# Optimization experiments

Hardware: AMD Instinct MI355X
Metric: run time of the kernel (lower is better)

## Reference

```python
import jax, jax.numpy as jnp
import numpy as np

N, M, D = 32768, 8192, 64

def setup_inputs() -> dict:
    key = jax.random.key(0)
    k1, k2, k3 = jax.random.split(key, 3)
    inputx = jax.random.normal(k1, (N, D), dtype=jnp.float32)
    y = jax.random.normal(k2, (M, D), dtype=jnp.float32)
    # psi is initialized to zeros in the module, but use random values so the
    # dual-variable subtraction actually affects the argmin/min.
    psi = jax.random.normal(k3, (M,), dtype=jnp.float32)
    return {"inputx": inputx, "y": y, "psi": psi}

def reference(inputx, y, psi):
    # cxy[i,j] = ||x_i||^2 + ||y_j||^2 - 2 <x_i, y_j>   (squared euclidean cost)
    x2 = jnp.sum(inputx * inputx, axis=1, keepdims=True)          # [N,1]
    y2 = jnp.sum(y * y, axis=1)[None, :]                          # [1,M]
    cxy = x2 + y2 - 2.0 * jnp.matmul(inputx, y.T)                 # [N,M]
    # semi-dual: mean_i min_j (c(x_i,y_j) - psi_j) + mean_j psi_j
    loss = jnp.mean(jnp.min(cxy - psi[None, :], axis=1)) + jnp.mean(psi)
    return loss
```

## Files before the change

### kernel.cpp

```cpp
#include <hip/hip_runtime.h>

#define N_ROWS 32768
#define M_COLS 8192
#define D_DIM  64
#define JC     8
#define BLOCK  256
#define ROWS_PER_BLOCK 256
#define CHUNK  (M_COLS / JC)
#define TJ     128
#define NTILE  (CHUNK / TJ)

typedef _Float16 v8h __attribute__((ext_vector_type(8)));
typedef _Float16 v4h __attribute__((ext_vector_type(4)));
typedef float    v4f __attribute__((ext_vector_type(4)));

__global__ __launch_bounds__(BLOCK) void prep_kernel(
    const float* __restrict__ y, const float* __restrict__ psi,
    _Float16* __restrict__ yh, float* __restrict__ th) {
    const int tid = threadIdx.x;
    const int j = blockIdx.x * 16 + (tid >> 4);
    const int n = tid & 15;
    const float4 v = *(const float4*)(y + (size_t)j * D_DIM + n * 4);
    float s = v.x * v.x + v.y * v.y + v.z * v.z + v.w * v.w;
    v4h hv = { (_Float16)v.x, (_Float16)v.y, (_Float16)v.z, (_Float16)v.w };
    *(v4h*)(yh + (size_t)j * D_DIM + n * 4) = hv;
#pragma unroll
    for (int m = 1; m < 16; m <<= 1) s += __shfl_xor(s, m, 64);
    if (n == 0) th[j] = 0.5f * (psi[j] - s);
}

__global__ __launch_bounds__(BLOCK) void partial_min_kernel(
    const float* __restrict__ x, const _Float16* __restrict__ yh,
    const float* __restrict__ th, float* __restrict__ part) {
    __shared__ __align__(16) _Float16 sY[2][TJ * D_DIM];

    const int tid  = threadIdx.x;
    const int lane = tid & 63, wave = tid >> 6;
    const int q = lane >> 4, n = lane & 15;
    const int jc    = blockIdx.y;
    const int jbase = jc * CHUNK;
    const int i_wave = blockIdx.x * ROWS_PER_BLOCK + wave * 64;

    v8h a[4][2];
#pragma unroll
    for (int g = 0; g < 4; ++g) {
        const float* px = x + (size_t)(i_wave + g * 16 + n) * D_DIM + q * 8;
#pragma unroll
        for (int c = 0; c < 2; ++c) {
            float4 f0 = *(const float4*)(px + c * 32);
            float4 f1 = *(const float4*)(px + c * 32 + 4);
            v8h av = { (_Float16)f0.x, (_Float16)f0.y, (_Float16)f0.z, (_Float16)f0.w,
                       (_Float16)f1.x, (_Float16)f1.y, (_Float16)f1.z, (_Float16)f1.w };
            a[g][c] = av;
        }
    }

    float maxs[4][4];
#pragma unroll
    for (int g = 0; g < 4; ++g)
#pragma unroll
        for (int r = 0; r < 4; ++r) maxs[g][r] = -INFINITY;

    auto stage = [&](int t, int b) {
#pragma unroll
        for (int k = 0; k < 4; ++k) {
            const int sIdx = (k * 4 + wave) * 64 + lane;
            const int row  = sIdx >> 3;
            const int c    = (sIdx & 7) ^ (row & 7);
            const _Float16* g = yh + (size_t)(jbase + t * TJ + row) * D_DIM + c * 8;
            __builtin_amdgcn_global_load_lds(
                (const __attribute__((address_space(1))) void*)g,
                (__attribute__((address_space(3))) void*)(&sY[b][(size_t)(k * 4 + wave) * 512]),
                16, 0, 0);
        }
    };

    stage(0, 0);
    __syncthreads();

    const int sl0 = q ^ (n & 7);

    for (int t = 0; t < NTILE; ++t) {
        const int cur = t & 1;
        if (t + 1 < NTILE) stage(t + 1, cur ^ 1);

        const _Float16* buf = &sY[cur][0];
        const float* pt = th + jbase + t * TJ + n;
#pragma unroll 2
        for (int ss = 0; ss < TJ / 16; ++ss) {
            const v8h b0 = *(const v8h*)(buf + (ss * 16 + n) * 64 + sl0 * 8);
            const v8h b1 = *(const v8h*)(buf + (ss * 16 + n) * 64 + (sl0 ^ 4) * 8);
            const float tv = pt[ss * 16];
            const v4f tv4 = { tv, tv, tv, tv };
#pragma unroll
            for (int g = 0; g < 4; ++g) {
                v4f acc = __builtin_amdgcn_mfma_f32_16x16x32_f16(a[g][0], b0, tv4, 0, 0, 0);
                acc     = __builtin_amdgcn_mfma_f32_16x16x32_f16(a[g][1], b1, acc, 0, 0, 0);
#pragma unroll
                for (int r = 0; r < 4; ++r)
                    maxs[g][r] = fmaxf(maxs[g][r], acc[r]);
            }
        }
        __syncthreads();
    }

#pragma unroll
    for (int g = 0; g < 4; ++g) {
#pragma unroll
        for (int r = 0; r < 4; ++r) {
            float v = maxs[g][r];
#pragma unroll
            for (int m = 1; m < 16; m <<= 1)
                v = fmaxf(v, __shfl_xor(v, m, 64));
            if (n == 0)
                part[(size_t)jc * N_ROWS + i_wave + g * 16 + q * 4 + r] = -2.f * v;
        }
    }
}

__global__ __launch_bounds__(BLOCK) void reduce_kernel(
    const float* __restrict__ part, const float* __restrict__ x,
    const float* __restrict__ psi, float* __restrict__ out) {
    const int tid = threadIdx.x;
    const int gt  = blockIdx.x * BLOCK + tid;
    float m = part[gt];
#pragma unroll
    for (int c = 1; c < JC; ++c)
        m = fminf(m, part[(size_t)c * N_ROWS + gt]);
    float s = m;
    const float4* xv = (const float4*)x;
    float x2 = 0.f;
#pragma unroll
    for (int k = 0; k < 16; ++k) {
        float4 v = xv[gt + k * 32768];
        x2 += v.x * v.x + v.y * v.y + v.z * v.z + v.w * v.w;
    }
    s = (s + x2) * (1.f / (float)N_ROWS);
    if (gt < M_COLS) s += psi[gt] * (1.f / (float)M_COLS);
    for (int off = 32; off > 0; off >>= 1) s += __shfl_down(s, off, 64);
    __shared__ float tmp[4];
    if ((tid & 63) == 0) tmp[tid >> 6] = s;
    __syncthreads();
    if (tid == 0) atomicAdd(out, tmp[0] + tmp[1] + tmp[2] + tmp[3]);
}

extern "C" void kernel_launch(void* const* d_in, const int* in_sizes, int n_in,
                              void* d_out, int out_size, void* d_ws, size_t ws_size,
                              hipStream_t stream) {
    const float* x   = (const float*)d_in[0];
    const float* y   = (const float*)d_in[1];
    const float* psi = (const float*)d_in[2];
    float* out = (float*)d_out;

    float* part = (float*)d_ws;
    float* th   = part + (size_t)JC * N_ROWS;
    _Float16* yh = (_Float16*)(th + M_COLS);

    hipMemsetAsync(out, 0, sizeof(float), stream);
    prep_kernel<<<M_COLS / 16, BLOCK, 0, stream>>>(y, psi, yh, th);
    partial_min_kernel<<<dim3(N_ROWS / ROWS_PER_BLOCK, JC), BLOCK, 0, stream>>>(x, yh, th, part);
    reduce_kernel<<<N_ROWS / BLOCK, BLOCK, 0, stream>>>(part, x, psi, out);
}
```

Measured before the change: 121.9 us.

## Double rows per wave, stage theta in LDS, fold output zeroing into prep

Each wave now processes 128 rows (8 MFMA groups) instead of 64, so every Y tile loaded into LDS feeds twice as many MFMAs and the block count halves. The per-column theta values are copied into LDS alongside Y through global_load_lds instead of being read from global memory inside the inner loop, and the inner loop is unrolled further. The hipMemsetAsync on the output is replaced by a store inside prep_kernel, which removes one launch. The cost is higher register pressure from doubled A fragments and accumulators, and only 512 blocks in the grid, which may reduce occupancy and leave some CUs idle.

```diff
diff --git a/kernel.cpp b/kernel.cpp
--- a/kernel.cpp
+++ b/kernel.cpp
@@ -5,7 +5,8 @@
 #define D_DIM  64
 #define JC     8
 #define BLOCK  256
-#define ROWS_PER_BLOCK 256
+#define GROUPS 8
+#define ROWS_PER_BLOCK 512
 #define CHUNK  (M_COLS / JC)
 #define TJ     128
 #define NTILE  (CHUNK / TJ)
@@ -16,8 +17,9 @@
 
 __global__ __launch_bounds__(BLOCK) void prep_kernel(
     const float* __restrict__ y, const float* __restrict__ psi,
-    _Float16* __restrict__ yh, float* __restrict__ th) {
+    _Float16* __restrict__ yh, float* __restrict__ th, float* __restrict__ out) {
     const int tid = threadIdx.x;
+    if (blockIdx.x == 0 && tid == 0) out[0] = 0.f;
     const int j = blockIdx.x * 16 + (tid >> 4);
     const int n = tid & 15;
     const float4 v = *(const float4*)(y + (size_t)j * D_DIM + n * 4);
@@ -33,17 +35,18 @@
     const float* __restrict__ x, const _Float16* __restrict__ yh,
     const float* __restrict__ th, float* __restrict__ part) {
     __shared__ __align__(16) _Float16 sY[2][TJ * D_DIM];
+    __shared__ __align__(16) float    sTh[2][TJ];
 
     const int tid  = threadIdx.x;
     const int lane = tid & 63, wave = tid >> 6;
     const int q = lane >> 4, n = lane & 15;
     const int jc    = blockIdx.y;
     const int jbase = jc * CHUNK;
-    const int i_wave = blockIdx.x * ROWS_PER_BLOCK + wave * 64;
+    const int i_wave = blockIdx.x * ROWS_PER_BLOCK + wave * 128;
 
-    v8h a[4][2];
+    v8h a[GROUPS][2];
 #pragma unroll
-    for (int g = 0; g < 4; ++g) {
+    for (int g = 0; g < GROUPS; ++g) {
         const float* px = x + (size_t)(i_wave + g * 16 + n) * D_DIM + q * 8;
 #pragma unroll
         for (int c = 0; c < 2; ++c) {
@@ -55,9 +58,9 @@
         }
     }
 
-    float maxs[4][4];
+    float maxs[GROUPS][4];
 #pragma unroll
-    for (int g = 0; g < 4; ++g)
+    for (int g = 0; g < GROUPS; ++g)
 #pragma unroll
         for (int r = 0; r < 4; ++r) maxs[g][r] = -INFINITY;
 
@@ -73,6 +76,13 @@
                 (__attribute__((address_space(3))) void*)(&sY[b][(size_t)(k * 4 + wave) * 512]),
                 16, 0, 0);
         }
+        if (wave == 0 && lane < 32) {
+            const float* gt_ = th + jbase + t * TJ + lane * 4;
+            __builtin_amdgcn_global_load_lds(
+                (const __attribute__((address_space(1))) void*)gt_,
+                (__attribute__((address_space(3))) void*)(&sTh[b][0]),
+                16, 0, 0);
+        }
     };
 
     stage(0, 0);
@@ -85,15 +95,15 @@
         if (t + 1 < NTILE) stage(t + 1, cur ^ 1);
 
         const _Float16* buf = &sY[cur][0];
-        const float* pt = th + jbase + t * TJ + n;
-#pragma unroll 2
+        const float* tbuf = &sTh[cur][0];
+#pragma unroll 4
         for (int ss = 0; ss < TJ / 16; ++ss) {
             const v8h b0 = *(const v8h*)(buf + (ss * 16 + n) * 64 + sl0 * 8);
             const v8h b1 = *(const v8h*)(buf + (ss * 16 + n) * 64 + (sl0 ^ 4) * 8);
-            const float tv = pt[ss * 16];
+            const float tv = tbuf[ss * 16 + n];
             const v4f tv4 = { tv, tv, tv, tv };
 #pragma unroll
-            for (int g = 0; g < 4; ++g) {
+            for (int g = 0; g < GROUPS; ++g) {
                 v4f acc = __builtin_amdgcn_mfma_f32_16x16x32_f16(a[g][0], b0, tv4, 0, 0, 0);
                 acc     = __builtin_amdgcn_mfma_f32_16x16x32_f16(a[g][1], b1, acc, 0, 0, 0);
 #pragma unroll
@@ -105,7 +115,7 @@
     }
 
 #pragma unroll
-    for (int g = 0; g < 4; ++g) {
+    for (int g = 0; g < GROUPS; ++g) {
 #pragma unroll
         for (int r = 0; r < 4; ++r) {
             float v = maxs[g][r];
@@ -156,8 +166,7 @@
     float* th   = part + (size_t)JC * N_ROWS;
     _Float16* yh = (_Float16*)(th + M_COLS);
 
-    hipMemsetAsync(out, 0, sizeof(float), stream);
-    prep_kernel<<<M_COLS / 16, BLOCK, 0, stream>>>(y, psi, yh, th);
+    prep_kernel<<<M_COLS / 16, BLOCK, 0, stream>>>(y, psi, yh, th, out);
     partial_min_kernel<<<dim3(N_ROWS / ROWS_PER_BLOCK, JC), BLOCK, 0, stream>>>(x, yh, th, part);
     reduce_kernel<<<N_ROWS / BLOCK, BLOCK, 0, stream>>>(part, x, psi, out);
 }
```

Measured after the change: 106.2 us. -12.9%, faster.
